# Performance work log

Hardware: AMD Instinct MI355X
Metric: run time of the kernel (lower is better)

## Reference

```python
import jax, jax.numpy as jnp
import numpy as np

H = 512

def _lstm_dir(seq, Wih, Whh, bih, bhh, reverse):
    # seq: [B,S,in]; Wih: [4H,in]; Whh: [4H,H]; biases [4H]
    B = seq.shape[0]
    xp = jnp.einsum('bsi,gi->bsg', seq, Wih) + bih  # precompute input projection [B,S,4H]
    h0 = jnp.zeros((B, H), seq.dtype)
    c0 = jnp.zeros((B, H), seq.dtype)

    def step(carry, xt):
        h, c = carry
        g = xt + h @ Whh.T + bhh
        i, f, gg, o = jnp.split(g, 4, axis=-1)
        c = jax.nn.sigmoid(f) * c + jax.nn.sigmoid(i) * jnp.tanh(gg)
        h = jax.nn.sigmoid(o) * jnp.tanh(c)
        return (h, c), h

    _, hs = jax.lax.scan(step, (h0, c0), jnp.swapaxes(xp, 0, 1), reverse=reverse)
    return jnp.swapaxes(hs, 0, 1)  # [B,S,H]


def setup_inputs() -> dict:
    key = jax.random.key(0)
    ks = jax.random.split(key, 24)
    B, S, E, V, C = 32, 512, 512, 32000, 2
    sc = 0.1
    d = {
        'x': jax.random.randint(ks[0], (B, S), 0, V, dtype=jnp.int32),
        'attention_mask': jnp.ones((B, S), dtype=jnp.int32),
        'emb': jax.random.normal(ks[1], (V, E), jnp.float32) * sc,
        'fc_W': jax.random.normal(ks[2], (C, 2 * H), jnp.float32) * sc,
        'fc_b': jax.random.normal(ks[3], (C,), jnp.float32) * sc,
    }
    i = 4
    for l, insz in [(0, E), (1, 2 * H)]:
        for dname in ('fwd', 'bwd'):
            d[f'{dname}_Wih{l}'] = jax.random.normal(ks[i], (4 * H, insz), jnp.float32) * sc; i += 1
            d[f'{dname}_Whh{l}'] = jax.random.normal(ks[i], (4 * H, H), jnp.float32) * sc; i += 1
            d[f'{dname}_bih{l}'] = jax.random.normal(ks[i], (4 * H,), jnp.float32) * sc; i += 1
            d[f'{dname}_bhh{l}'] = jax.random.normal(ks[i], (4 * H,), jnp.float32) * sc; i += 1
    return d


def reference(x, attention_mask, emb, fc_W, fc_b,
              fwd_Wih0, fwd_Whh0, fwd_bih0, fwd_bhh0,
              bwd_Wih0, bwd_Whh0, bwd_bih0, bwd_bhh0,
              fwd_Wih1, fwd_Whh1, fwd_bih1, fwd_bhh1,
              bwd_Wih1, bwd_Whh1, bwd_bih1, bwd_bhh1):
    out = emb[x]  # [B,S,E]
    layers = [
        ((fwd_Wih0, fwd_Whh0, fwd_bih0, fwd_bhh0), (bwd_Wih0, bwd_Whh0, bwd_bih0, bwd_bhh0)),
        ((fwd_Wih1, fwd_Whh1, fwd_bih1, fwd_bhh1), (bwd_Wih1, bwd_Whh1, bwd_bih1, bwd_bhh1)),
    ]
    for fw, bw in layers:
        f = _lstm_dir(out, *fw, reverse=False)
        b = _lstm_dir(out, *bw, reverse=True)
        out = jnp.concatenate([f, b], axis=-1)  # [B,S,2H]
        # dropout is identity in eval mode
    mask = attention_mask.astype(out.dtype)
    pooled = (out * mask[..., None]).sum(axis=1) / jnp.clip(mask.sum(axis=1, keepdims=True), 1e-9)
    logits = pooled @ fc_W.T + fc_b
    return logits
```

## Files before the change

### kernel.cpp

```cpp
#include <hip/hip_runtime.h>

typedef unsigned short u16;
typedef unsigned int   u32;
typedef unsigned long long u64;
typedef __attribute__((ext_vector_type(8))) short bf16x8;
typedef __attribute__((ext_vector_type(4))) float f32x4;

__device__ __forceinline__ u16 f2bf(float f) {
    u32 u; __builtin_memcpy(&u, &f, 4);
    u32 r = (u + 0x7FFFu + ((u >> 16) & 1u)) >> 16;
    return (u16)r;
}
__device__ __forceinline__ float bf2f(u16 h) {
    u32 u = ((u32)h) << 16; float f; __builtin_memcpy(&f, &u, 4); return f;
}
__device__ __forceinline__ float sigmoidf(float x) { return 1.f / (1.f + __expf(-x)); }
__device__ __forceinline__ float tanh_safe(float x) {
    float e = __expf(-2.f * fabsf(x));
    float t = (1.f - e) / (1.f + e);
    return x >= 0.f ? t : -t;
}

__global__ __launch_bounds__(256) void castk2(const float* __restrict__ s, u16* __restrict__ hi,
                                              u16* __restrict__ lo, int n) {
    int i = blockIdx.x * 256 + threadIdx.x;
    if (i < n) {
        float f = s[i];
        u16 h = f2bf(f);
        hi[i] = h;
        lo[i] = f2bf(f - bf2f(h));
    }
}

__global__ __launch_bounds__(256) void embed_cast(const int* __restrict__ x, const float* __restrict__ emb,
                                                  u16* __restrict__ x0) {
    int m = blockIdx.x;
    int idx = x[m];
    const float2* src = (const float2*)(emb + (size_t)idx * 512);
    u16* dst = x0 + (size_t)m * 512;
    int t = threadIdx.x;
    float2 v = src[t];
    dst[t * 2]     = f2bf(v.x);
    dst[t * 2 + 1] = f2bf(v.y);
}

__global__ __launch_bounds__(256) void gemm_bt(const u16* __restrict__ A, const u16* __restrict__ Bhi,
                                               const u16* __restrict__ Blo,
                                               u16* __restrict__ C, int M, int N, int K) {
    __shared__ __align__(16) u16 sA[128 * 32];
    __shared__ __align__(16) u16 sBh[128 * 32];
    __shared__ __align__(16) u16 sBl[128 * 32];
    const int tid  = threadIdx.x;
    const int lane = tid & 63, wave = tid >> 6;
    const int m0 = blockIdx.y * 128, n0 = blockIdx.x * 128;
    const int wm = (wave >> 1) * 64, wn = (wave & 1) * 64;
    f32x4 acc[4][4] = {};

    const int r0 = tid >> 2, c8 = (tid & 3) * 8;
    const int r1 = r0 + 64;
    const u16* Ap   = A   + (size_t)(m0 + r0) * K + c8;
    const u16* Ap2  = A   + (size_t)(m0 + r1) * K + c8;
    const u16* Bhp  = Bhi + (size_t)(n0 + r0) * K + c8;
    const u16* Bhp2 = Bhi + (size_t)(n0 + r1) * K + c8;
    const u16* Blp  = Blo + (size_t)(n0 + r0) * K + c8;
    const u16* Blp2 = Blo + (size_t)(n0 + r1) * K + c8;

    uint4 ra0, ra1, rh0, rh1, rl0, rl1;
    ra0 = *(const uint4*)(Ap);   ra1 = *(const uint4*)(Ap2);
    rh0 = *(const uint4*)(Bhp);  rh1 = *(const uint4*)(Bhp2);
    rl0 = *(const uint4*)(Blp);  rl1 = *(const uint4*)(Blp2);

    for (int kk = 0; kk < K; kk += 32) {
        __syncthreads();
        *(uint4*)(sA  + tid * 8)        = ra0;
        *(uint4*)(sA  + 2048 + tid * 8) = ra1;
        *(uint4*)(sBh + tid * 8)        = rh0;
        *(uint4*)(sBh + 2048 + tid * 8) = rh1;
        *(uint4*)(sBl + tid * 8)        = rl0;
        *(uint4*)(sBl + 2048 + tid * 8) = rl1;
        int kn = kk + 32;
        if (kn < K) {
            ra0 = *(const uint4*)(Ap + kn);   ra1 = *(const uint4*)(Ap2 + kn);
            rh0 = *(const uint4*)(Bhp + kn);  rh1 = *(const uint4*)(Bhp2 + kn);
            rl0 = *(const uint4*)(Blp + kn);  rl1 = *(const uint4*)(Blp2 + kn);
        }
        __syncthreads();
        bf16x8 av[4], bh[4], bl[4];
#pragma unroll
        for (int i = 0; i < 4; ++i) {
            av[i] = *(const bf16x8*)(sA  + (wm + i * 16 + (lane & 15)) * 32 + (lane >> 4) * 8);
            bh[i] = *(const bf16x8*)(sBh + (wn + i * 16 + (lane & 15)) * 32 + (lane >> 4) * 8);
            bl[i] = *(const bf16x8*)(sBl + (wn + i * 16 + (lane & 15)) * 32 + (lane >> 4) * 8);
        }
#pragma unroll
        for (int i = 0; i < 4; ++i)
#pragma unroll
            for (int j = 0; j < 4; ++j) {
                acc[i][j] = __builtin_amdgcn_mfma_f32_16x16x32_bf16(av[i], bh[j], acc[i][j], 0, 0, 0);
                acc[i][j] = __builtin_amdgcn_mfma_f32_16x16x32_bf16(av[i], bl[j], acc[i][j], 0, 0, 0);
            }
    }
#pragma unroll
    for (int i = 0; i < 4; ++i) {
        int m = m0 + wm + i * 16 + ((lane >> 4) << 2);
#pragma unroll
        for (int j = 0; j < 4; ++j) {
            int n = n0 + wn + j * 16 + (lane & 15);
#pragma unroll
            for (int rr = 0; rr < 4; ++rr)
                C[(size_t)(m + rr) * N + n] = f2bf(acc[i][j][rr]);
        }
    }
}

template <int LAYER>
__global__ __launch_bounds__(256, 1) void lstm_rec(
    const u16* __restrict__ xp_f, const u16* __restrict__ xp_b,
    const u16* __restrict__ whh_f_hi, const u16* __restrict__ whh_f_lo,
    const u16* __restrict__ whh_b_hi, const u16* __restrict__ whh_b_lo,
    const float* __restrict__ bih_f, const float* __restrict__ bhh_f,
    const float* __restrict__ bih_b, const float* __restrict__ bhh_b,
    u16* __restrict__ out0, float* __restrict__ pooled, const int* __restrict__ mask,
    u16* hbuf, u32* cnt)
{
    const int HP = 524;
    __shared__ __align__(16) u16  sHhi[32 * 524];
    __shared__ __align__(16) u16  sHlo[32 * 524];
    __shared__ __align__(16) float sG[32 * 33];

    const int tid = threadIdx.x;
    const int dir = blockIdx.x >> 6;
    const int slice = blockIdx.x & 63;
    const u16* xp     = dir ? xp_b : xp_f;
    const u16* whhH   = dir ? whh_b_hi : whh_f_hi;
    const u16* whhL   = dir ? whh_b_lo : whh_f_lo;
    const float* bih  = dir ? bih_b : bih_f;
    const float* bhh  = dir ? bhh_b : bhh_f;
    u16* hbD = hbuf + dir * 65536;
    u32* myFlags = cnt + dir * 256;

    const int wave = tid >> 6, lane = tid & 63;
    const int wm = (wave >> 1) * 16;
    const int wn = (wave & 1) * 16;
    bf16x8 wfragH[16], wfragL[16];
    {
        int n = wn + (lane & 15);
        int q = n >> 3, rr = n & 7;
        size_t rowoff = (size_t)(q * 512 + slice * 8 + rr) * 512 + (lane >> 4) * 8;
        const u16* wrh = whhH + rowoff;
        const u16* wrl = whhL + rowoff;
#pragma unroll
        for (int k2 = 0; k2 < 16; ++k2) {
            wfragH[k2] = *(const bf16x8*)(wrh + k2 * 32);
            wfragL[k2] = *(const bf16x8*)(wrl + k2 * 32);
        }
    }
    const int b = tid >> 3, r = tid & 7;
    float bias[4];
#pragma unroll
    for (int q = 0; q < 4; ++q) {
        int g = q * 512 + slice * 8 + r;
        bias[q] = bih[g] + bhh[g];
    }
    float cstate = 0.f, pool = 0.f;
    const int aoff = (wm + (lane & 15)) * HP + (lane >> 4) * 8;
    const int gRow = wm + ((lane >> 4) << 2), gCol = wn + (lane & 15);
    const int srow = tid >> 3, sc = tid & 7;
    const u16* xpBase = xp + (size_t)(b * 512) * 2048 + slice * 8 + r;

    for (int t = 0; t < 512; ++t) {
        const int tt = dir ? (511 - t) : t;
        const u16* xrow = xpBase + (size_t)tt * 2048;
        u16 xv0 = xrow[0], xv1 = xrow[512], xv2 = xrow[1024], xv3 = xrow[1536];
        if (t > 0 && tid < 64) {
            const u32 tgt = (u32)t;
            const u64* fp = (const u64*)(myFlags + tid * 4);
            for (;;) {
                u64 f01 = __hip_atomic_load(fp,     __ATOMIC_RELAXED, __HIP_MEMORY_SCOPE_AGENT);
                u64 f23 = __hip_atomic_load(fp + 1, __ATOMIC_RELAXED, __HIP_MEMORY_SCOPE_AGENT);
                int ok = ((u32)f01 >= tgt) & ((u32)(f01 >> 32) >= tgt) &
                         ((u32)f23 >= tgt) & ((u32)(f23 >> 32) >= tgt);
                if (__all(ok)) break;
                __builtin_amdgcn_s_sleep(1);
            }
        }
        __syncthreads();
        if (t > 0) {
            const u16* hp = hbD + ((t - 1) & 1) * 32768 + srow * 512;
            const u16* lp = hp + 16384;
            u16* dhi = sHhi + srow * HP;
            u16* dlo = sHlo + srow * HP;
            u64 rh[16], rl[16];
#pragma unroll
            for (int j = 0; j < 8; ++j) {
                int ch = sc + 8 * j;
                rh[2*j]   = __hip_atomic_load((const u64*)(hp + ch * 8),     __ATOMIC_RELAXED, __HIP_MEMORY_SCOPE_AGENT);
                rh[2*j+1] = __hip_atomic_load((const u64*)(hp + ch * 8) + 1, __ATOMIC_RELAXED, __HIP_MEMORY_SCOPE_AGENT);
                rl[2*j]   = __hip_atomic_load((const u64*)(lp + ch * 8),     __ATOMIC_RELAXED, __HIP_MEMORY_SCOPE_AGENT);
                rl[2*j+1] = __hip_atomic_load((const u64*)(lp + ch * 8) + 1, __ATOMIC_RELAXED, __HIP_MEMORY_SCOPE_AGENT);
            }
#pragma unroll
            for (int j = 0; j < 8; ++j) {
                int ch = sc + 8 * j;
                *(u64*)(dhi + ch * 8)     = rh[2*j];
                *(u64*)(dhi + ch * 8 + 4) = rh[2*j+1];
                *(u64*)(dlo + ch * 8)     = rl[2*j];
                *(u64*)(dlo + ch * 8 + 4) = rl[2*j+1];
            }
        }
        __syncthreads();
        f32x4 ac0 = {}, ac1 = {}, ac2 = {};
        if (t > 0) {
#pragma unroll
            for (int k2 = 0; k2 < 16; ++k2) {
                bf16x8 ah = *(const bf16x8*)(sHhi + aoff + k2 * 32);
                bf16x8 al = *(const bf16x8*)(sHlo + aoff + k2 * 32);
                ac0 = __builtin_amdgcn_mfma_f32_16x16x32_bf16(ah, wfragH[k2], ac0, 0, 0, 0);
                ac1 = __builtin_amdgcn_mfma_f32_16x16x32_bf16(al, wfragH[k2], ac1, 0, 0, 0);
                ac2 = __builtin_amdgcn_mfma_f32_16x16x32_bf16(ah, wfragL[k2], ac2, 0, 0, 0);
            }
        }
#pragma unroll
        for (int rr = 0; rr < 4; ++rr) sG[(gRow + rr) * 33 + gCol] = ac0[rr] + ac1[rr] + ac2[rr];
        __syncthreads();
        {
            float gq[4];
            gq[0] = sG[b * 33 + 0 * 8 + r] + bf2f(xv0) + bias[0];
            gq[1] = sG[b * 33 + 1 * 8 + r] + bf2f(xv1) + bias[1];
            gq[2] = sG[b * 33 + 2 * 8 + r] + bf2f(xv2) + bias[2];
            gq[3] = sG[b * 33 + 3 * 8 + r] + bf2f(xv3) + bias[3];
            float ig = sigmoidf(gq[0]), fg = sigmoidf(gq[1]);
            float gg = tanh_safe(gq[2]), og = sigmoidf(gq[3]);
            cstate = fg * cstate + ig * gg;
            float h = og * tanh_safe(cstate);
            u16 hh = f2bf(h);
            u16 hl = f2bf(h - bf2f(hh));
            if (LAYER == 0) {
                out0[((size_t)(b * 512 + tt)) * 1024 + dir * 512 + slice * 8 + r] = hh;
            } else {
                pool += h * (float)mask[b * 512 + tt];
            }
            u16* gh = hbD + (t & 1) * 32768 + b * 512 + slice * 8 + r;
            __hip_atomic_store(gh,         hh, __ATOMIC_RELAXED, __HIP_MEMORY_SCOPE_AGENT);
            __hip_atomic_store(gh + 16384, hl, __ATOMIC_RELAXED, __HIP_MEMORY_SCOPE_AGENT);
            asm volatile("s_waitcnt vmcnt(0)" ::: "memory");
            if ((tid & 63) == 0)
                __hip_atomic_store(myFlags + slice * 4 + wave, (u32)(t + 1),
                                   __ATOMIC_RELAXED, __HIP_MEMORY_SCOPE_AGENT);
        }
    }
    if (LAYER == 1)
        pooled[(size_t)b * 1024 + dir * 512 + slice * 8 + r] = pool;
}

__global__ __launch_bounds__(256) void final_fc(const float* __restrict__ pooled, const int* __restrict__ mask,
                                                const float* __restrict__ fcW, const float* __restrict__ fcb,
                                                float* __restrict__ out) {
    __shared__ float red[256];
    int tid = threadIdx.x;
    int pair = tid & 63, kc = tid >> 6;
    int b = pair >> 1, c = pair & 1;
    float s = 0.f;
    for (int k = kc * 256; k < kc * 256 + 256; ++k)
        s += pooled[b * 1024 + k] * fcW[c * 1024 + k];
    red[tid] = s;
    __syncthreads();
    if (kc == 0) {
        float tot = red[pair] + red[64 + pair] + red[128 + pair] + red[192 + pair];
        float ms = 0.f;
        for (int t = 0; t < 512; ++t) ms += (float)mask[b * 512 + t];
        ms = fmaxf(ms, 1e-9f);
        out[b * 2 + c] = tot / ms + fcb[c];
    }
}

extern "C" void kernel_launch(void* const* d_in, const int* in_sizes, int n_in,
                              void* d_out, int out_size, void* d_ws, size_t ws_size,
                              hipStream_t stream) {
    (void)in_sizes; (void)n_in; (void)out_size; (void)ws_size;
    const int*   x     = (const int*)d_in[0];
    const int*   amask = (const int*)d_in[1];
    const float* emb   = (const float*)d_in[2];
    const float* fcW   = (const float*)d_in[3];
    const float* fcb   = (const float*)d_in[4];
    const float* fWih0 = (const float*)d_in[5];
    const float* fWhh0 = (const float*)d_in[6];
    const float* fbih0 = (const float*)d_in[7];
    const float* fbhh0 = (const float*)d_in[8];
    const float* bWih0 = (const float*)d_in[9];
    const float* bWhh0 = (const float*)d_in[10];
    const float* bbih0 = (const float*)d_in[11];
    const float* bbhh0 = (const float*)d_in[12];
    const float* fWih1 = (const float*)d_in[13];
    const float* fWhh1 = (const float*)d_in[14];
    const float* fbih1 = (const float*)d_in[15];
    const float* fbhh1 = (const float*)d_in[16];
    const float* bWih1 = (const float*)d_in[17];
    const float* bWhh1 = (const float*)d_in[18];
    const float* bbih1 = (const float*)d_in[19];
    const float* bbhh1 = (const float*)d_in[20];

    char* ws = (char*)d_ws;
    size_t off = 0;
    auto alloc = [&](size_t bytes) { void* p = ws + off; off += (bytes + 1023) & ~(size_t)1023; return p; };
    u16* x0    = (u16*)alloc((size_t)16384 * 512 * 2);
    u16* xpf   = (u16*)alloc((size_t)16384 * 2048 * 2);
    u16* xpb   = (u16*)alloc((size_t)16384 * 2048 * 2);
    u16* out0  = (u16*)alloc((size_t)16384 * 1024 * 2);
    u16* wih0fH = (u16*)alloc((size_t)2048 * 512 * 2);
    u16* wih0fL = (u16*)alloc((size_t)2048 * 512 * 2);
    u16* wih0bH = (u16*)alloc((size_t)2048 * 512 * 2);
    u16* wih0bL = (u16*)alloc((size_t)2048 * 512 * 2);
    u16* whh0fH = (u16*)alloc((size_t)2048 * 512 * 2);
    u16* whh0fL = (u16*)alloc((size_t)2048 * 512 * 2);
    u16* whh0bH = (u16*)alloc((size_t)2048 * 512 * 2);
    u16* whh0bL = (u16*)alloc((size_t)2048 * 512 * 2);
    u16* wih1fH = (u16*)alloc((size_t)2048 * 1024 * 2);
    u16* wih1fL = (u16*)alloc((size_t)2048 * 1024 * 2);
    u16* wih1bH = (u16*)alloc((size_t)2048 * 1024 * 2);
    u16* wih1bL = (u16*)alloc((size_t)2048 * 1024 * 2);
    u16* whh1fH = (u16*)alloc((size_t)2048 * 512 * 2);
    u16* whh1fL = (u16*)alloc((size_t)2048 * 512 * 2);
    u16* whh1bH = (u16*)alloc((size_t)2048 * 512 * 2);
    u16* whh1bL = (u16*)alloc((size_t)2048 * 512 * 2);
    float* pooled = (float*)alloc((size_t)32 * 1024 * 4);
    u16* hbuf  = (u16*)alloc((size_t)2 * 2 * 2 * 32 * 512 * 2);
    u32* cnt   = (u32*)alloc(4096);

    hipMemsetAsync(cnt, 0, 4096, stream);

    const int NW0 = 2048 * 512, NW1 = 2048 * 1024;
    castk2<<<dim3((NW0 + 255) / 256), 256, 0, stream>>>(fWih0, wih0fH, wih0fL, NW0);
    castk2<<<dim3((NW0 + 255) / 256), 256, 0, stream>>>(bWih0, wih0bH, wih0bL, NW0);
    castk2<<<dim3((NW0 + 255) / 256), 256, 0, stream>>>(fWhh0, whh0fH, whh0fL, NW0);
    castk2<<<dim3((NW0 + 255) / 256), 256, 0, stream>>>(bWhh0, whh0bH, whh0bL, NW0);
    castk2<<<dim3((NW1 + 255) / 256), 256, 0, stream>>>(fWih1, wih1fH, wih1fL, NW1);
    castk2<<<dim3((NW1 + 255) / 256), 256, 0, stream>>>(bWih1, wih1bH, wih1bL, NW1);
    castk2<<<dim3((NW0 + 255) / 256), 256, 0, stream>>>(fWhh1, whh1fH, whh1fL, NW0);
    castk2<<<dim3((NW0 + 255) / 256), 256, 0, stream>>>(bWhh1, whh1bH, whh1bL, NW0);

    embed_cast<<<dim3(16384), 256, 0, stream>>>(x, emb, x0);

    gemm_bt<<<dim3(16, 128), 256, 0, stream>>>(x0, wih0fH, wih0fL, xpf, 16384, 2048, 512);
    gemm_bt<<<dim3(16, 128), 256, 0, stream>>>(x0, wih0bH, wih0bL, xpb, 16384, 2048, 512);
    lstm_rec<0><<<dim3(128), 256, 0, stream>>>(xpf, xpb, whh0fH, whh0fL, whh0bH, whh0bL,
                                               fbih0, fbhh0, bbih0, bbhh0,
                                               out0, nullptr, nullptr, hbuf, cnt);
    gemm_bt<<<dim3(16, 128), 256, 0, stream>>>(out0, wih1fH, wih1fL, xpf, 16384, 2048, 1024);
    gemm_bt<<<dim3(16, 128), 256, 0, stream>>>(out0, wih1bH, wih1bL, xpb, 16384, 2048, 1024);
    lstm_rec<1><<<dim3(128), 256, 0, stream>>>(xpf, xpb, whh1fH, whh1fL, whh1bH, whh1bL,
                                               fbih1, fbhh1, bbih1, bbhh1,
                                               nullptr, pooled, amask, hbuf, cnt + 512);

    final_fc<<<dim3(1), 256, 0, stream>>>(pooled, amask, fcW, fcb, (float*)d_out);
}
```

Measured before the change: 6.385 ms.

## Split recurrent matmul along K across waves, load h directly into MFMA fragments

The recurrent h·Whh product is repartitioned so each wave covers a quarter of the K dimension for all 32 batch rows and 32 gate columns, instead of a 16x16 output tile over the full K. Each wave loads its h fragments straight from global memory into registers, which removes the LDS staging of h and one __syncthreads per timestep. Partial sums from the four waves are written to a per-wave LDS buffer and reduced in the gate step. The cost is a four-way LDS reduction per step and more global load traffic per wave, in exchange for a shorter serial critical path per timestep.

Measured after the change: 8.774 ms. 1.37x slower.

```diff
diff --git a/kernel.cpp b/kernel.cpp
--- a/kernel.cpp
+++ b/kernel.cpp
@@ -19,6 +19,9 @@
     float e = __expf(-2.f * fabsf(x));
     float t = (1.f - e) / (1.f + e);
     return x >= 0.f ? t : -t;
+}
+__device__ __forceinline__ bf16x8 mk8(u64 a, u64 b) {
+    union { u64 u[2]; bf16x8 v; } x; x.u[0] = a; x.u[1] = b; return x.v;
 }
 
 __global__ __launch_bounds__(256) void castk2(const float* __restrict__ s, u16* __restrict__ hi,
@@ -123,10 +126,7 @@
     u16* __restrict__ out0, float* __restrict__ pooled, const int* __restrict__ mask,
     u16* hbuf, u32* cnt)
 {
-    const int HP = 524;
-    __shared__ __align__(16) u16  sHhi[32 * 524];
-    __shared__ __align__(16) u16  sHlo[32 * 524];
-    __shared__ __align__(16) float sG[32 * 33];
+    __shared__ __align__(16) float sGp[4][32][34];
 
     const int tid = threadIdx.x;
     const int dir = blockIdx.x >> 6;
@@ -140,19 +140,18 @@
     u32* myFlags = cnt + dir * 256;
 
     const int wave = tid >> 6, lane = tid & 63;
-    const int wm = (wave >> 1) * 16;
-    const int wn = (wave & 1) * 16;
-    bf16x8 wfragH[16], wfragL[16];
-    {
-        int n = wn + (lane & 15);
+    const int l15 = lane & 15, lk8 = (lane >> 4) * 8;
+    bf16x8 wfH[2][4], wfL[2][4];
+#pragma unroll
+    for (int c = 0; c < 2; ++c) {
+        int n = c * 16 + l15;
         int q = n >> 3, rr = n & 7;
-        size_t rowoff = (size_t)(q * 512 + slice * 8 + rr) * 512 + (lane >> 4) * 8;
-        const u16* wrh = whhH + rowoff;
-        const u16* wrl = whhL + rowoff;
-#pragma unroll
-        for (int k2 = 0; k2 < 16; ++k2) {
-            wfragH[k2] = *(const bf16x8*)(wrh + k2 * 32);
-            wfragL[k2] = *(const bf16x8*)(wrl + k2 * 32);
+        size_t rowoff = (size_t)(q * 512 + slice * 8 + rr) * 512;
+#pragma unroll
+        for (int k2l = 0; k2l < 4; ++k2l) {
+            size_t off = rowoff + (size_t)((wave * 4 + k2l) * 32 + lk8);
+            wfH[c][k2l] = *(const bf16x8*)(whhH + off);
+            wfL[c][k2l] = *(const bf16x8*)(whhL + off);
         }
     }
     const int b = tid >> 3, r = tid & 7;
@@ -163,9 +162,8 @@
         bias[q] = bih[g] + bhh[g];
     }
     float cstate = 0.f, pool = 0.f;
-    const int aoff = (wm + (lane & 15)) * HP + (lane >> 4) * 8;
-    const int gRow = wm + ((lane >> 4) << 2), gCol = wn + (lane & 15);
-    const int srow = tid >> 3, sc = tid & 7;
+    const int kcol = wave * 128 + lk8;
+    const int gRow = (lane >> 4) << 2;
     const u16* xpBase = xp + (size_t)(b * 512) * 2048 + slice * 8 + r;
 
     for (int t = 0; t < 512; ++t) {
@@ -185,50 +183,53 @@
             }
         }
         __syncthreads();
+        f32x4 acc[2][2][3] = {};
         if (t > 0) {
-            const u16* hp = hbD + ((t - 1) & 1) * 32768 + srow * 512;
-            const u16* lp = hp + 16384;
-            u16* dhi = sHhi + srow * HP;
-            u16* dlo = sHlo + srow * HP;
-            u64 rh[16], rl[16];
-#pragma unroll
-            for (int j = 0; j < 8; ++j) {
-                int ch = sc + 8 * j;
-                rh[2*j]   = __hip_atomic_load((const u64*)(hp + ch * 8),     __ATOMIC_RELAXED, __HIP_MEMORY_SCOPE_AGENT);
-                rh[2*j+1] = __hip_atomic_load((const u64*)(hp + ch * 8) + 1, __ATOMIC_RELAXED, __HIP_MEMORY_SCOPE_AGENT);
-                rl[2*j]   = __hip_atomic_load((const u64*)(lp + ch * 8),     __ATOMIC_RELAXED, __HIP_MEMORY_SCOPE_AGENT);
-                rl[2*j+1] = __hip_atomic_load((const u64*)(lp + ch * 8) + 1, __ATOMIC_RELAXED, __HIP_MEMORY_SCOPE_AGENT);
-            }
-#pragma unroll
-            for (int j = 0; j < 8; ++j) {
-                int ch = sc + 8 * j;
-                *(u64*)(dhi + ch * 8)     = rh[2*j];
-                *(u64*)(dhi + ch * 8 + 4) = rh[2*j+1];
-                *(u64*)(dlo + ch * 8)     = rl[2*j];
-                *(u64*)(dlo + ch * 8 + 4) = rl[2*j+1];
-            }
-        }
-        __syncthreads();
-        f32x4 ac0 = {}, ac1 = {}, ac2 = {};
-        if (t > 0) {
-#pragma unroll
-            for (int k2 = 0; k2 < 16; ++k2) {
-                bf16x8 ah = *(const bf16x8*)(sHhi + aoff + k2 * 32);
-                bf16x8 al = *(const bf16x8*)(sHlo + aoff + k2 * 32);
-                ac0 = __builtin_amdgcn_mfma_f32_16x16x32_bf16(ah, wfragH[k2], ac0, 0, 0, 0);
-                ac1 = __builtin_amdgcn_mfma_f32_16x16x32_bf16(al, wfragH[k2], ac1, 0, 0, 0);
-                ac2 = __builtin_amdgcn_mfma_f32_16x16x32_bf16(ah, wfragL[k2], ac2, 0, 0, 0);
-            }
-        }
-#pragma unroll
-        for (int rr = 0; rr < 4; ++rr) sG[(gRow + rr) * 33 + gCol] = ac0[rr] + ac1[rr] + ac2[rr];
+            const u16* hp = hbD + ((t - 1) & 1) * 32768;
+            u64 rh[4][2][2], rl[4][2][2];
+#pragma unroll
+            for (int k2l = 0; k2l < 4; ++k2l)
+#pragma unroll
+                for (int m = 0; m < 2; ++m) {
+                    const u16* base = hp + (m * 16 + l15) * 512 + kcol + k2l * 32;
+                    rh[k2l][m][0] = __hip_atomic_load((const u64*)base,             __ATOMIC_RELAXED, __HIP_MEMORY_SCOPE_AGENT);
+                    rh[k2l][m][1] = __hip_atomic_load((const u64*)base + 1,         __ATOMIC_RELAXED, __HIP_MEMORY_SCOPE_AGENT);
+                    rl[k2l][m][0] = __hip_atomic_load((const u64*)(base + 16384),     __ATOMIC_RELAXED, __HIP_MEMORY_SCOPE_AGENT);
+                    rl[k2l][m][1] = __hip_atomic_load((const u64*)(base + 16384) + 1, __ATOMIC_RELAXED, __HIP_MEMORY_SCOPE_AGENT);
+                }
+#pragma unroll
+            for (int k2l = 0; k2l < 4; ++k2l)
+#pragma unroll
+                for (int m = 0; m < 2; ++m) {
+                    bf16x8 ah = mk8(rh[k2l][m][0], rh[k2l][m][1]);
+                    bf16x8 al = mk8(rl[k2l][m][0], rl[k2l][m][1]);
+#pragma unroll
+                    for (int c = 0; c < 2; ++c) {
+                        acc[m][c][0] = __builtin_amdgcn_mfma_f32_16x16x32_bf16(ah, wfH[c][k2l], acc[m][c][0], 0, 0, 0);
+                        acc[m][c][1] = __builtin_amdgcn_mfma_f32_16x16x32_bf16(al, wfH[c][k2l], acc[m][c][1], 0, 0, 0);
+                        acc[m][c][2] = __builtin_amdgcn_mfma_f32_16x16x32_bf16(ah, wfL[c][k2l], acc[m][c][2], 0, 0, 0);
+                    }
+                }
+        }
+#pragma unroll
+        for (int m = 0; m < 2; ++m)
+#pragma unroll
+            for (int c = 0; c < 2; ++c)
+#pragma unroll
+                for (int rr = 0; rr < 4; ++rr)
+                    sGp[wave][m * 16 + gRow + rr][c * 16 + l15] =
+                        acc[m][c][0][rr] + acc[m][c][1][rr] + acc[m][c][2][rr];
         __syncthreads();
         {
             float gq[4];
-            gq[0] = sG[b * 33 + 0 * 8 + r] + bf2f(xv0) + bias[0];
-            gq[1] = sG[b * 33 + 1 * 8 + r] + bf2f(xv1) + bias[1];
-            gq[2] = sG[b * 33 + 2 * 8 + r] + bf2f(xv2) + bias[2];
-            gq[3] = sG[b * 33 + 3 * 8 + r] + bf2f(xv3) + bias[3];
+#pragma unroll
+            for (int q = 0; q < 4; ++q)
+                gq[q] = sGp[0][b][q * 8 + r] + sGp[1][b][q * 8 + r]
+                      + sGp[2][b][q * 8 + r] + sGp[3][b][q * 8 + r];
+            gq[0] += bf2f(xv0) + bias[0];
+            gq[1] += bf2f(xv1) + bias[1];
+            gq[2] += bf2f(xv2) + bias[2];
+            gq[3] += bf2f(xv3) + bias[3];
             float ig = sigmoidf(gq[0]), fg = sigmoidf(gq[1]);
             float gg = tanh_safe(gq[2]), og = sigmoidf(gq[3]);
             cstate = fg * cstate + ig * gg;
@@ -244,7 +245,7 @@
             __hip_atomic_store(gh,         hh, __ATOMIC_RELAXED, __HIP_MEMORY_SCOPE_AGENT);
             __hip_atomic_store(gh + 16384, hl, __ATOMIC_RELAXED, __HIP_MEMORY_SCOPE_AGENT);
             asm volatile("s_waitcnt vmcnt(0)" ::: "memory");
-            if ((tid & 63) == 0)
+            if (lane == 0)
                 __hip_atomic_store(myFlags + slice * 4 + wave, (u32)(t + 1),
                                    __ATOMIC_RELAXED, __HIP_MEMORY_SCOPE_AGENT);
         }
```
